# Performance work log

Hardware: AMD Instinct MI355X
Metric: run time of the kernel (lower is better)

Reference implementation:

```python
import jax, jax.numpy as jnp
import numpy as np

WINDOW = 7
NUM_HEADS = 12
DIM = 384


def _relative_position_index(ws):
    coords_h = np.arange(ws)
    coords_w = np.arange(ws)
    coords = np.stack(np.meshgrid(coords_h, coords_w, indexing='ij'))  # [2,ws,ws]
    coords_flatten = coords.transpose(1, 2, 0).reshape(-1, 2)          # [ws*ws,2]
    rel = coords_flatten[:, None, :] - coords_flatten[None, :, :]      # [N,N,2]
    rel[:, :, 0] += ws - 1
    rel[:, :, 1] += ws - 1
    rel[:, :, 0] *= 2 * ws - 1
    return rel.sum(-1).astype(np.int32)                                # [N,N]


def setup_inputs() -> dict:
    key = jax.random.key(0)
    ks = jax.random.split(key, 8)
    B_, N, C, H = 4096, WINDOW * WINDOW, DIM, NUM_HEADS
    x = jax.random.normal(ks[0], (B_, N, C), dtype=jnp.float32)
    mask = jax.random.normal(ks[1], (1, 1, N, N), dtype=jnp.float32)
    qkv_w = jax.random.normal(ks[2], (C, 3 * C), dtype=jnp.float32) * 0.02
    qkv_b = jnp.zeros((3 * C,), dtype=jnp.float32)
    proj_w = jax.random.normal(ks[3], (C, C), dtype=jnp.float32) * 0.02
    proj_b = jnp.zeros((C,), dtype=jnp.float32)
    bias_table = jax.random.normal(ks[4], ((2 * WINDOW - 1) ** 2, H), dtype=jnp.float32) * 0.02
    rel_index = jnp.asarray(_relative_position_index(WINDOW))  # int32 [N,N]
    return {"x": x, "mask": mask, "qkv_w": qkv_w, "qkv_b": qkv_b,
            "proj_w": proj_w, "proj_b": proj_b, "bias_table": bias_table,
            "rel_index": rel_index}


def reference(x, mask, qkv_w, qkv_b, proj_w, proj_b, bias_table, rel_index):
    B_, N, C = x.shape
    H = NUM_HEADS
    hd = C // H
    scale = hd ** (-0.5)
    # qkv projection -> [3, B_, H, N, hd]
    qkv = (x @ qkv_w + qkv_b).reshape(B_, N, 3, H, hd).transpose(2, 0, 3, 1, 4)
    q, k, v = qkv[0], qkv[1], qkv[2]
    attn = jnp.einsum('bhnd,bhmd->bhnm', q, k) * scale  # [B_,H,N,N]
    # gathered relative position bias: [N,N,H] -> [H,N,N]
    bias = bias_table[rel_index].transpose(2, 0, 1)
    attn = attn + bias[None] + mask
    attn = jax.nn.softmax(attn, axis=-1)
    out = jnp.einsum('bhnm,bhmd->bhnd', attn, v)        # [B_,H,N,hd]
    out = out.transpose(0, 2, 1, 3).reshape(B_, N, C)
    return out @ proj_w + proj_b
```

## Files before the change

### kernel.cpp

```cpp
#include <hip/hip_runtime.h>
#include <hip/hip_bf16.h>
#include <stdint.h>

typedef unsigned short u16;
typedef __bf16 bf16x8 __attribute__((ext_vector_type(8)));
typedef float f32x4 __attribute__((ext_vector_type(4)));

#define NWIN 4096
#define NTOK 49
#define CDIM 384
#define NHEAD 12
#define HD 32
#define MROWS (NWIN * NTOK)
#define QKVN (3 * CDIM)
#define SCALE 0.17677669529663689f

__device__ __forceinline__ u16 f2bf(float f) {
  uint32_t u = __float_as_uint(f);
  u += 0x7fff + ((u >> 16) & 1);
  return (u16)(u >> 16);
}

__device__ __forceinline__ void gload_lds16(const void* g, void* l) {
  __builtin_amdgcn_global_load_lds(
      (const __attribute__((address_space(1))) unsigned int*)g,
      (__attribute__((address_space(3))) unsigned int*)l, 16, 0, 0);
}


__global__ __launch_bounds__(256) void cvt_x_kernel(const float* __restrict__ x,
                                                    u16* __restrict__ xb, int n4) {
  int i = blockIdx.x * blockDim.x + threadIdx.x;
  int stride = gridDim.x * blockDim.x;
  for (; i < n4; i += stride) {
    float4 v = ((const float4*)x)[i];
    ushort4 o;
    o.x = f2bf(v.x); o.y = f2bf(v.y); o.z = f2bf(v.z); o.w = f2bf(v.w);
    ((ushort4*)xb)[i] = o;
  }
}

__global__ __launch_bounds__(256) void cvt_wT_kernel(const float* __restrict__ w,
                                                     u16* __restrict__ wT, int K, int N) {
  int i = blockIdx.x * blockDim.x + threadIdx.x;
  if (i >= K * N) return;
  int n = i / K, k = i - n * K;
  wT[i] = f2bf(w[k * N + n]);
}

__global__ __launch_bounds__(256) void build_bias_kernel(const float* __restrict__ bt,
                                                         const int* __restrict__ ri,
                                                         const float* __restrict__ mask,
                                                         float* __restrict__ bias12p) {
  int i = blockIdx.x * blockDim.x + threadIdx.x;
  if (i >= NHEAD * 64 * 64) return;
  int h = i >> 12, r = (i >> 6) & 63, c = i & 63;
  float v = 0.f;
  if (r < NTOK && c < NTOK) v = bt[ri[r * NTOK + c] * NHEAD + h] + mask[r * NTOK + c];
  bias12p[i] = v;
}


template <int MODE>
__global__ __launch_bounds__(256) void gemm128(const u16* __restrict__ A,
                                               const u16* __restrict__ BT,
                                               const float* __restrict__ bias,
                                               float* __restrict__ outF,
                                               u16* __restrict__ q_ws,
                                               u16* __restrict__ k_ws,
                                               u16* __restrict__ vT_ws,
                                               int K, int n_tiles) {
  __shared__ __align__(16) u16 As[128 * 64];
  __shared__ __align__(16) u16 Bs[128 * 64];
  const int tid = threadIdx.x;
  const int wave = tid >> 6, lane = tid & 63;
  const int mt = blockIdx.x / n_tiles, nt = blockIdx.x % n_tiles;
  const int m0 = mt << 7, n0 = nt << 7;
  const int fr = lane & 15, fg = lane >> 4;
  const int wr = (wave >> 1) << 6, wc = (wave & 1) << 6;

  f32x4 acc[4][4] = {};

  for (int k0 = 0; k0 < K; k0 += 64) {
#pragma unroll
    for (int it = 0; it < 4; ++it) {
      const int c = it * 256 + tid;
      const int row = c >> 3, col8 = c & 7;
      gload_lds16(A + (size_t)(m0 + row) * K + k0 + col8 * 8, &As[c * 8]);
    }
#pragma unroll
    for (int it = 0; it < 4; ++it) {
      const int c = it * 256 + tid;
      const int row = c >> 3, col8 = c & 7;
      gload_lds16(BT + (size_t)(n0 + row) * K + k0 + col8 * 8, &Bs[c * 8]);
    }
    asm volatile("s_waitcnt vmcnt(0)" ::: "memory");
    __syncthreads();
#pragma unroll
    for (int kk = 0; kk < 2; ++kk) {
      bf16x8 av[4], bv[4];
#pragma unroll
      for (int i = 0; i < 4; ++i)
        av[i] = *(const bf16x8*)&As[(wr + i * 16 + fr) * 64 + kk * 32 + fg * 8];
#pragma unroll
      for (int i = 0; i < 4; ++i)
        bv[i] = *(const bf16x8*)&Bs[(wc + i * 16 + fr) * 64 + kk * 32 + fg * 8];
#pragma unroll
      for (int i = 0; i < 4; ++i)
#pragma unroll
        for (int j = 0; j < 4; ++j)
          acc[i][j] = __builtin_amdgcn_mfma_f32_16x16x32_bf16(av[i], bv[j], acc[i][j], 0, 0, 0);
    }
    __syncthreads();
  }

#pragma unroll
  for (int j = 0; j < 4; ++j) {
    const int col_g = n0 + wc + j * 16 + fr;
    const float bvadd = bias[col_g];
    if (MODE == 0) {
      const int s = col_g / CDIM;
      const int cr = col_g - s * CDIM;
      const int h = cr >> 5, d = cr & 31;
#pragma unroll
      for (int i = 0; i < 4; ++i) {
#pragma unroll
        for (int r = 0; r < 4; ++r) {
          const int row_g = m0 + wr + i * 16 + fg * 4 + r;
          const int b = row_g / NTOK, n = row_g - b * NTOK;
          const float v = acc[i][j][r] + bvadd;
          const size_t bh = (size_t)b * NHEAD + h;
          if (s == 0)      q_ws[(bh * NTOK + n) * HD + d] = f2bf(v * SCALE);
          else if (s == 1) k_ws[(bh * NTOK + n) * HD + d] = f2bf(v);
          else             vT_ws[(bh * HD + d) * 64 + n] = f2bf(v);
        }
      }
    } else {
#pragma unroll
      for (int i = 0; i < 4; ++i) {
#pragma unroll
        for (int r = 0; r < 4; ++r) {
          const int row_g = m0 + wr + i * 16 + fg * 4 + r;
          outF[(size_t)row_g * CDIM + col_g] = acc[i][j][r] + bvadd;
        }
      }
    }
  }
}


__global__ __launch_bounds__(64) void attn_kernel(const u16* __restrict__ q_ws,
                                                  const u16* __restrict__ k_ws,
                                                  const u16* __restrict__ vT_ws,
                                                  const float* __restrict__ bias12p,
                                                  u16* __restrict__ att_ws) {
  __shared__ __align__(16) float S[64 * 68];
  __shared__ __align__(16) u16 P[64 * 72];
  const int bh = blockIdx.x;
  const int b = bh / NHEAD, h = bh - b * NHEAD;
  const int lane = threadIdx.x;
  const int fr = lane & 15, fg = lane >> 4;
  const u16* qp = q_ws + (size_t)bh * NTOK * HD;
  const u16* kp = k_ws + (size_t)bh * NTOK * HD;
  const u16* vp = vT_ws + (size_t)bh * HD * 64;

  bf16x8 aq[4], bk[4];
#pragma unroll
  for (int i = 0; i < 4; ++i) {
    int m = i * 16 + fr;
    m = m < NTOK ? m : NTOK - 1;
    aq[i] = *(const bf16x8*)&qp[m * HD + fg * 8];
    bk[i] = *(const bf16x8*)&kp[m * HD + fg * 8];
  }
  f32x4 sacc[4][4] = {};
#pragma unroll
  for (int i = 0; i < 4; ++i)
#pragma unroll
    for (int j = 0; j < 4; ++j)
      sacc[i][j] = __builtin_amdgcn_mfma_f32_16x16x32_bf16(aq[i], bk[j], sacc[i][j], 0, 0, 0);

  const float* bp = bias12p + h * 64 * 64;
#pragma unroll
  for (int i = 0; i < 4; ++i)
#pragma unroll
    for (int j = 0; j < 4; ++j)
#pragma unroll
      for (int r = 0; r < 4; ++r) {
        const int row = i * 16 + fg * 4 + r, col = j * 16 + fr;
        S[row * 68 + col] = sacc[i][j][r] + bp[row * 64 + col];
      }
  __syncthreads();

  {
    const int r = lane;
    if (r < NTOK) {
      float mx = -1e30f;
      for (int j = 0; j < NTOK; ++j) mx = fmaxf(mx, S[r * 68 + j]);
      float sum = 0.f;
      for (int j = 0; j < NTOK; ++j) {
        float e = __expf(S[r * 68 + j] - mx);
        sum += e;
        S[r * 68 + j] = e;
      }
      const float inv = 1.f / sum;
      for (int j = 0; j < NTOK; ++j) P[r * 72 + j] = f2bf(S[r * 68 + j] * inv);
      for (int j = NTOK; j < 64; ++j) P[r * 72 + j] = 0;
    } else {
      for (int j = 0; j < 64; ++j) P[r * 72 + j] = 0;
    }
  }
  __syncthreads();

  f32x4 oacc[4][2] = {};
#pragma unroll
  for (int kt = 0; kt < 2; ++kt) {
    bf16x8 ap[4], bv[2];
#pragma unroll
    for (int i = 0; i < 4; ++i)
      ap[i] = *(const bf16x8*)&P[(i * 16 + fr) * 72 + kt * 32 + fg * 8];
#pragma unroll
    for (int n2 = 0; n2 < 2; ++n2)
      bv[n2] = *(const bf16x8*)&vp[(n2 * 16 + fr) * 64 + kt * 32 + fg * 8];
#pragma unroll
    for (int i = 0; i < 4; ++i)
#pragma unroll
      for (int n2 = 0; n2 < 2; ++n2)
        oacc[i][n2] = __builtin_amdgcn_mfma_f32_16x16x32_bf16(ap[i], bv[n2], oacc[i][n2], 0, 0, 0);
  }
  u16* ao = att_ws + ((size_t)b * NTOK) * CDIM + h * HD;
#pragma unroll
  for (int i = 0; i < 4; ++i)
#pragma unroll
    for (int n2 = 0; n2 < 2; ++n2)
#pragma unroll
      for (int r = 0; r < 4; ++r) {
        const int row = i * 16 + fg * 4 + r, col = n2 * 16 + fr;
        if (row < NTOK) ao[(size_t)row * CDIM + col] = f2bf(oacc[i][n2][r]);
      }
}


extern "C" void kernel_launch(void* const* d_in, const int* in_sizes, int n_in,
                              void* d_out, int out_size, void* d_ws, size_t ws_size,
                              hipStream_t stream) {
  (void)in_sizes; (void)n_in; (void)out_size; (void)ws_size;
  const float* x      = (const float*)d_in[0];
  const float* mask   = (const float*)d_in[1];
  const float* qkv_w  = (const float*)d_in[2];
  const float* qkv_b  = (const float*)d_in[3];
  const float* proj_w = (const float*)d_in[4];
  const float* proj_b = (const float*)d_in[5];
  const float* btab   = (const float*)d_in[6];
  const int*   ridx   = (const int*)d_in[7];
  float* out = (float*)d_out;

  char* ws = (char*)d_ws;
  size_t off = 0;
  auto alloc = [&](size_t bytes) {
    char* p = ws + off;
    off = (off + bytes + 255) & ~(size_t)255;
    return p;
  };
  u16* q_ws    = (u16*)alloc((size_t)NWIN * NHEAD * NTOK * HD * 2);
  u16* k_ws    = (u16*)alloc((size_t)NWIN * NHEAD * NTOK * HD * 2);
  u16* vT_ws   = (u16*)alloc((size_t)NWIN * NHEAD * HD * 64 * 2);
  u16* att_ws  = (u16*)alloc((size_t)MROWS * CDIM * 2);
  u16* qkvWT   = (u16*)alloc((size_t)QKVN * CDIM * 2);
  u16* projWT  = (u16*)alloc((size_t)CDIM * CDIM * 2);
  float* bias12p = (float*)alloc((size_t)NHEAD * 64 * 64 * 4);

  u16* x_bf = (u16*)d_out;

  cvt_x_kernel<<<4096, 256, 0, stream>>>(x, x_bf, MROWS * CDIM / 4);
  cvt_wT_kernel<<<(QKVN * CDIM + 255) / 256, 256, 0, stream>>>(qkv_w, qkvWT, CDIM, QKVN);
  cvt_wT_kernel<<<(CDIM * CDIM + 255) / 256, 256, 0, stream>>>(proj_w, projWT, CDIM, CDIM);
  build_bias_kernel<<<(NHEAD * 64 * 64 + 255) / 256, 256, 0, stream>>>(btab, ridx, mask, bias12p);

  gemm128<0><<<(MROWS / 128) * (QKVN / 128), 256, 0, stream>>>(
      x_bf, qkvWT, qkv_b, nullptr, q_ws, k_ws, vT_ws, CDIM, QKVN / 128);

  attn_kernel<<<NWIN * NHEAD, 64, 0, stream>>>(q_ws, k_ws, vT_ws, bias12p, att_ws);

  gemm128<1><<<(MROWS / 128) * (CDIM / 128), 256, 0, stream>>>(
      att_ws, projWT, proj_b, out, nullptr, nullptr, nullptr, CDIM, CDIM / 128);
}
```

Measured before the change: 1.384 ms.

## Double-buffer GEMM LDS loads with XOR swizzle, block remap, and padded softmax scratch

The GEMM kernel now double-buffers its A and B tiles in LDS, issuing the next K-slice's global-to-LDS loads before running the MFMAs on the current slice. It also applies an XOR swizzle to the LDS layout to cut bank conflicts, remaps block IDs in groups of eight, and raises wave priority around the MFMA burst. In the attention kernel the score scratch row stride changes from 68 to 65 so the per-row softmax loop reads LDS without bank conflicts. The risks are the doubled LDS footprint lowering occupancy, and the removed vmcnt wait, which leaves correctness of the async loads dependent on the barrier alone.

```diff
diff --git a/kernel.cpp b/kernel.cpp
--- a/kernel.cpp
+++ b/kernel.cpp
@@ -70,48 +70,74 @@
                                                u16* __restrict__ k_ws,
                                                u16* __restrict__ vT_ws,
                                                int K, int n_tiles) {
-  __shared__ __align__(16) u16 As[128 * 64];
-  __shared__ __align__(16) u16 Bs[128 * 64];
+  __shared__ __align__(16) u16 As[2][128 * 64];
+  __shared__ __align__(16) u16 Bs[2][128 * 64];
   const int tid = threadIdx.x;
   const int wave = tid >> 6, lane = tid & 63;
-  const int mt = blockIdx.x / n_tiles, nt = blockIdx.x % n_tiles;
-  const int m0 = mt << 7, n0 = nt << 7;
+
+  const int nwg = gridDim.x;
+  int bid = blockIdx.x;
+  bid = (bid & 7) * (nwg >> 3) + (bid >> 3);
+
+  const int mt = bid / n_tiles, ntile = bid - mt * n_tiles;
+  const int m0 = mt << 7, n0 = ntile << 7;
   const int fr = lane & 15, fg = lane >> 4;
   const int wr = (wave >> 1) << 6, wc = (wave & 1) << 6;
 
   f32x4 acc[4][4] = {};
 
-  for (int k0 = 0; k0 < K; k0 += 64) {
+  auto stage = [&](int k0s, int bufi) {
 #pragma unroll
     for (int it = 0; it < 4; ++it) {
       const int c = it * 256 + tid;
       const int row = c >> 3, col8 = c & 7;
-      gload_lds16(A + (size_t)(m0 + row) * K + k0 + col8 * 8, &As[c * 8]);
+      const int scol = ((col8 ^ (row & 7)) << 3);
+      gload_lds16(A + (size_t)(m0 + row) * K + k0s + scol, &As[bufi][c * 8]);
     }
 #pragma unroll
     for (int it = 0; it < 4; ++it) {
       const int c = it * 256 + tid;
       const int row = c >> 3, col8 = c & 7;
-      gload_lds16(BT + (size_t)(n0 + row) * K + k0 + col8 * 8, &Bs[c * 8]);
-    }
-    asm volatile("s_waitcnt vmcnt(0)" ::: "memory");
-    __syncthreads();
+      const int scol = ((col8 ^ (row & 7)) << 3);
+      gload_lds16(BT + (size_t)(n0 + row) * K + k0s + scol, &Bs[bufi][c * 8]);
+    }
+  };
+
+  const int nt = K >> 6;
+  int cur = 0;
+
+  stage(0, 0);
+  __syncthreads();
+
+  for (int t = 0; t < nt; ++t) {
+    if (t + 1 < nt) stage((t + 1) << 6, cur ^ 1);
+
 #pragma unroll
     for (int kk = 0; kk < 2; ++kk) {
       bf16x8 av[4], bv[4];
 #pragma unroll
-      for (int i = 0; i < 4; ++i)
-        av[i] = *(const bf16x8*)&As[(wr + i * 16 + fr) * 64 + kk * 32 + fg * 8];
-#pragma unroll
-      for (int i = 0; i < 4; ++i)
-        bv[i] = *(const bf16x8*)&Bs[(wc + i * 16 + fr) * 64 + kk * 32 + fg * 8];
+      for (int i = 0; i < 4; ++i) {
+        const int row = wr + i * 16 + fr;
+        const int swz = ((kk << 2) | fg) ^ (fr & 7);
+        av[i] = *(const bf16x8*)((const char*)&As[cur][0] + (size_t)row * 128 + (swz << 4));
+      }
+#pragma unroll
+      for (int i = 0; i < 4; ++i) {
+        const int row = wc + i * 16 + fr;
+        const int swz = ((kk << 2) | fg) ^ (fr & 7);
+        bv[i] = *(const bf16x8*)((const char*)&Bs[cur][0] + (size_t)row * 128 + (swz << 4));
+      }
+      __builtin_amdgcn_s_setprio(1);
 #pragma unroll
       for (int i = 0; i < 4; ++i)
 #pragma unroll
         for (int j = 0; j < 4; ++j)
           acc[i][j] = __builtin_amdgcn_mfma_f32_16x16x32_bf16(av[i], bv[j], acc[i][j], 0, 0, 0);
-    }
-    __syncthreads();
+      __builtin_amdgcn_s_setprio(0);
+    }
+
+    if (t + 1 < nt) __syncthreads();
+    cur ^= 1;
   }
 
 #pragma unroll
@@ -154,7 +180,7 @@
                                                   const u16* __restrict__ vT_ws,
                                                   const float* __restrict__ bias12p,
                                                   u16* __restrict__ att_ws) {
-  __shared__ __align__(16) float S[64 * 68];
+  __shared__ __align__(16) float S[64 * 65];
   __shared__ __align__(16) u16 P[64 * 72];
   const int bh = blockIdx.x;
   const int b = bh / NHEAD, h = bh - b * NHEAD;
@@ -187,7 +213,7 @@
 #pragma unroll
       for (int r = 0; r < 4; ++r) {
         const int row = i * 16 + fg * 4 + r, col = j * 16 + fr;
-        S[row * 68 + col] = sacc[i][j][r] + bp[row * 64 + col];
+        S[row * 65 + col] = sacc[i][j][r] + bp[row * 64 + col];
       }
   __syncthreads();
 
@@ -195,15 +221,15 @@
     const int r = lane;
     if (r < NTOK) {
       float mx = -1e30f;
-      for (int j = 0; j < NTOK; ++j) mx = fmaxf(mx, S[r * 68 + j]);
+      for (int j = 0; j < NTOK; ++j) mx = fmaxf(mx, S[r * 65 + j]);
       float sum = 0.f;
       for (int j = 0; j < NTOK; ++j) {
-        float e = __expf(S[r * 68 + j] - mx);
+        float e = __expf(S[r * 65 + j] - mx);
         sum += e;
-        S[r * 68 + j] = e;
+        S[r * 65 + j] = e;
       }
       const float inv = 1.f / sum;
-      for (int j = 0; j < NTOK; ++j) P[r * 72 + j] = f2bf(S[r * 68 + j] * inv);
+      for (int j = 0; j < NTOK; ++j) P[r * 72 + j] = f2bf(S[r * 65 + j] * inv);
       for (int j = NTOK; j < 64; ++j) P[r * 72 + j] = 0;
     } else {
       for (int j = 0; j < 64; ++j) P[r * 72 + j] = 0;
```

New measurement: 1.317 ms. -4.9%, faster.
